# Kernel optimization log

Measured on AMD Instinct MI355X. Metric: run time of the kernel, lower is better.

Reference implementation:

```python
import jax, jax.numpy as jnp
import numpy as np

B, A, N_IN, N_HID, N_OUT, MAX_Z = 2048, 96, 128, 64, 1, 100
SHIFT = float(np.log(2.0))

def ssp(x):
    # shifted softplus: softplus(x) - log(2)
    return jax.nn.softplus(x) - SHIFT

def setup_inputs() -> dict:
    key = jax.random.key(0)
    ks = jax.random.split(key, 8)
    rep = jax.random.normal(ks[0], (B, A, N_IN), dtype=jnp.float32)
    atomic_numbers = jax.random.randint(ks[1], (B, A), 0, MAX_Z)
    atom_mask = jnp.ones((B, A), dtype=jnp.float32)
    s1 = 1.0 / np.sqrt(N_IN)
    s2 = 1.0 / np.sqrt(N_HID)
    W1 = jax.random.uniform(ks[2], (N_IN, N_HID), jnp.float32, -s1, s1)
    b1 = jax.random.uniform(ks[3], (N_HID,), jnp.float32, -s1, s1)
    W2 = jax.random.uniform(ks[4], (N_HID, N_OUT), jnp.float32, -s2, s2)
    b2 = jax.random.uniform(ks[5], (N_OUT,), jnp.float32, -s2, s2)
    atomref_table = jax.random.normal(ks[6], (MAX_Z, N_OUT), dtype=jnp.float32) * 0.1
    atomref_table = atomref_table.at[0].set(0.0)  # mask-atom reference is zero
    mean = jnp.array([0.0], dtype=jnp.float32)
    stddev = jnp.array([1.0], dtype=jnp.float32)
    return {"representation": rep, "atomic_numbers": atomic_numbers,
            "atom_mask": atom_mask, "W1": W1, "b1": b1, "W2": W2, "b2": b2,
            "atomref_table": atomref_table, "mean": mean, "stddev": stddev}

def reference(representation, atomic_numbers, atom_mask, W1, b1, W2, b2,
              atomref_table, mean, stddev):
    # per-atom MLP: [B,A,n_in] -> [B,A,n_out]
    h = ssp(jnp.einsum('bai,ih->bah', representation, W1) + b1)
    yi = jnp.einsum('bah,ho->bao', h, W2) + b2
    # standardize (ScaleShift): y * stddev + mean
    yi = yi * stddev + mean
    # atomref embedding lookup and add
    yi = yi + atomref_table[atomic_numbers]  # [B,A,n_out]
    # masked sum aggregation over atoms (Aggregate axis=1, mean=False)
    y = jnp.sum(yi * atom_mask[..., None], axis=1)  # [B,n_out]
    return y
```

## Files before the change

### kernel.cpp

```cpp
#include <hip/hip_runtime.h>

#define BB 2048
#define AA 96
#define NIN 128
#define NHID 64
#define MI 3

typedef __attribute__((ext_vector_type(8))) short bf16x8;
typedef __attribute__((ext_vector_type(4))) float f32x4;

static __device__ __forceinline__ unsigned f2bf(float x) {
    unsigned u = __builtin_bit_cast(unsigned, x);
    return (u + 0x7FFFu + ((u >> 16) & 1u)) >> 16;
}
static __device__ __forceinline__ unsigned cvt_pk(float a, float b) {
    return f2bf(a) | (f2bf(b) << 16);
}

__global__ __launch_bounds__(256) void atomwise_kernel(
    const float* __restrict__ rep,
    const int*   __restrict__ zs,
    const float* __restrict__ mask,
    const float* __restrict__ w1,
    const float* __restrict__ b1,
    const float* __restrict__ w2,
    const float* __restrict__ b2,
    const float* __restrict__ aref,
    const float* __restrict__ mean,
    const float* __restrict__ stddev,
    float* __restrict__ out)
{
    __shared__ bf16x8 w1f[1024];
    __shared__ float  b1s[NHID], w2s[NHID];

    const int tid  = threadIdx.x;
    const int lane = tid & 63;
    const int wv   = tid >> 6;
    const int nl   = lane & 15;
    const int quad = lane >> 4;

    #pragma unroll
    for (int f = 0; f < 4; ++f) {
        const int fid = tid + f * 256;
        const int l2  = fid & 63;
        const int st  = fid >> 6;
        const int k0  = (st >> 2) * 32 + (l2 >> 4) * 8;
        const int n   = (st & 3) * 16 + (l2 & 15);
        union { bf16x8 v; unsigned u[4]; } fb;
        #pragma unroll
        for (int jp = 0; jp < 4; ++jp)
            fb.u[jp] = cvt_pk(w1[(k0 + 2 * jp) * NHID + n],
                              w1[(k0 + 2 * jp + 1) * NHID + n]);
        w1f[fid] = fb.v;
    }
    if (tid < NHID) { b1s[tid] = b1[tid]; w2s[tid] = w2[tid]; }
    __syncthreads();

    const float sdv  = stddev[0];
    const float cadd = fmaf(b2[0], sdv, mean[0]);
    const float LOG2E = 1.4426950408889634f;
    const float LN2   = 0.6931471805599453f;

    const int wid = blockIdx.x * 4 + wv;

    #pragma unroll 1
    for (int mt = 0; mt < MI; ++mt) {
        const int atom0 = (wid * MI + mt) * 16;
        const float* rowp = rep + (size_t)(atom0 + nl) * NIN + quad * 8;

        f32x4 acc[4];
        #pragma unroll
        for (int t = 0; t < 4; ++t) acc[t] = (f32x4){0.f, 0.f, 0.f, 0.f};

        #pragma unroll 1
        for (int s = 0; s < 4; ++s) {
            const float4 a0 = *(const float4*)(rowp + s * 32);
            const float4 a1 = *(const float4*)(rowp + s * 32 + 4);
            union { bf16x8 v; unsigned u[4]; } fa;
            fa.u[0] = cvt_pk(a0.x, a0.y);
            fa.u[1] = cvt_pk(a0.z, a0.w);
            fa.u[2] = cvt_pk(a1.x, a1.y);
            fa.u[3] = cvt_pk(a1.z, a1.w);
            const bf16x8* fr = &w1f[s * 256 + lane];
            #pragma unroll
            for (int t = 0; t < 4; ++t)
                acc[t] = __builtin_amdgcn_mfma_f32_16x16x32_bf16(fa.v, fr[t * 64], acc[t], 0, 0, 0);
        }

        float v[4];
        #pragma unroll
        for (int r = 0; r < 4; ++r) {
            float p = 0.f;
            #pragma unroll
            for (int t = 0; t < 4; ++t) {
                float x  = acc[t][r] + b1s[t * 16 + nl];
                float ax = fabsf(x);
                float em = exp2f(-ax * LOG2E);
                float sp = fmaxf(x, 0.f) + log2f(1.f + em) * LN2;
                p = fmaf(sp - LN2, w2s[t * 16 + nl], p);
            }
            p += __shfl_xor(p, 1); p += __shfl_xor(p, 2);
            p += __shfl_xor(p, 4); p += __shfl_xor(p, 8);
            v[r] = p;
        }
        if (nl == 0) {
            float ssum = 0.f;
            #pragma unroll
            for (int r = 0; r < 4; ++r) {
                const int ag = atom0 + quad * 4 + r;
                const float yi = fmaf(v[r], sdv, cadd) + aref[zs[ag]];
                ssum += mask[ag] * yi;
            }
            ssum += __shfl_xor(ssum, 16);
            ssum += __shfl_xor(ssum, 32);
            if (lane == 0) atomicAdd(out + atom0 / AA, ssum);
        }
    }
}

extern "C" void kernel_launch(void* const* d_in, const int* in_sizes, int n_in,
                              void* d_out, int out_size, void* d_ws, size_t ws_size,
                              hipStream_t stream) {
    const float* rep    = (const float*)d_in[0];
    const int*   zs     = (const int*)  d_in[1];
    const float* mask   = (const float*)d_in[2];
    const float* w1     = (const float*)d_in[3];
    const float* b1     = (const float*)d_in[4];
    const float* w2     = (const float*)d_in[5];
    const float* b2     = (const float*)d_in[6];
    const float* aref   = (const float*)d_in[7];
    const float* mean   = (const float*)d_in[8];
    const float* stddev = (const float*)d_in[9];
    float* out = (float*)d_out;

    (void)hipMemsetAsync(out, 0, (size_t)out_size * sizeof(float), stream);

    const int atoms  = BB * AA;
    const int blocks = atoms / (4 * 16 * MI);
    atomwise_kernel<<<dim3(blocks), dim3(256), 0, stream>>>(
        rep, zs, mask, w1, b1, w2, b2, aref, mean, stddev, out);
}
```

Measured before the change: 166.1 us.

## Hoist all row loads before MFMA loop, coalesce W1 staging, and use smaller per-wave tile

All eight float4 loads of a 16-atom tile are now issued up front and the K loop is fully unrolled, so the memory latency of the representation reads overlaps instead of being serialized per K step. W1 staging to LDS now reads contiguous float4s and scatters bf16 halves into the fragment layout, replacing strided scalar global reads. MI drops from 3 to 2, so the grid has more blocks and more waves in flight. The cost is more VGPRs for the prefetched rows and a larger share of per-block W1 staging overhead.

```diff
diff --git a/kernel.cpp b/kernel.cpp
--- a/kernel.cpp
+++ b/kernel.cpp
@@ -4,7 +4,7 @@
 #define AA 96
 #define NIN 128
 #define NHID 64
-#define MI 3
+#define MI 2
 
 typedef __attribute__((ext_vector_type(8))) short bf16x8;
 typedef __attribute__((ext_vector_type(4))) float f32x4;
@@ -39,21 +39,26 @@
     const int nl   = lane & 15;
     const int quad = lane >> 4;
 
-    #pragma unroll
-    for (int f = 0; f < 4; ++f) {
-        const int fid = tid + f * 256;
-        const int l2  = fid & 63;
-        const int st  = fid >> 6;
-        const int k0  = (st >> 2) * 32 + (l2 >> 4) * 8;
-        const int n   = (st & 3) * 16 + (l2 & 15);
-        union { bf16x8 v; unsigned u[4]; } fb;
+    {
+        unsigned short* w1h = (unsigned short*)w1f;
+        const float4* w14 = (const float4*)w1;
         #pragma unroll
-        for (int jp = 0; jp < 4; ++jp)
-            fb.u[jp] = cvt_pk(w1[(k0 + 2 * jp) * NHID + n],
-                              w1[(k0 + 2 * jp + 1) * NHID + n]);
-        w1f[fid] = fb.v;
+        for (int i = 0; i < 8; ++i) {
+            const int idx = tid + i * 256;
+            const float4 v = w14[idx];
+            const int k  = idx >> 4;
+            const int n0 = (idx & 15) * 4;
+            const int s = k >> 5, qd = (k >> 3) & 3, jp = (k & 7) >> 1, hf = k & 1;
+            const int t = n0 >> 4;
+            const int base = ((s * 4 + t) * 64 + qd * 16 + (n0 & 15)) * 8 + jp * 2 + hf;
+            w1h[base     ] = (unsigned short)f2bf(v.x);
+            w1h[base +  8] = (unsigned short)f2bf(v.y);
+            w1h[base + 16] = (unsigned short)f2bf(v.z);
+            w1h[base + 24] = (unsigned short)f2bf(v.w);
+        }
+        if (tid < NHID)            b1s[tid] = b1[tid];
+        else if (tid < 2 * NHID)   w2s[tid - NHID] = w2[tid - NHID];
     }
-    if (tid < NHID) { b1s[tid] = b1[tid]; w2s[tid] = w2[tid]; }
     __syncthreads();
 
     const float sdv  = stddev[0];
@@ -68,19 +73,24 @@
         const int atom0 = (wid * MI + mt) * 16;
         const float* rowp = rep + (size_t)(atom0 + nl) * NIN + quad * 8;
 
+        float4 q[8];
+        #pragma unroll
+        for (int s = 0; s < 4; ++s) {
+            q[2 * s]     = *(const float4*)(rowp + s * 32);
+            q[2 * s + 1] = *(const float4*)(rowp + s * 32 + 4);
+        }
+
         f32x4 acc[4];
         #pragma unroll
         for (int t = 0; t < 4; ++t) acc[t] = (f32x4){0.f, 0.f, 0.f, 0.f};
 
-        #pragma unroll 1
+        #pragma unroll
         for (int s = 0; s < 4; ++s) {
-            const float4 a0 = *(const float4*)(rowp + s * 32);
-            const float4 a1 = *(const float4*)(rowp + s * 32 + 4);
             union { bf16x8 v; unsigned u[4]; } fa;
-            fa.u[0] = cvt_pk(a0.x, a0.y);
-            fa.u[1] = cvt_pk(a0.z, a0.w);
-            fa.u[2] = cvt_pk(a1.x, a1.y);
-            fa.u[3] = cvt_pk(a1.z, a1.w);
+            fa.u[0] = cvt_pk(q[2 * s].x,     q[2 * s].y);
+            fa.u[1] = cvt_pk(q[2 * s].z,     q[2 * s].w);
+            fa.u[2] = cvt_pk(q[2 * s + 1].x, q[2 * s + 1].y);
+            fa.u[3] = cvt_pk(q[2 * s + 1].z, q[2 * s + 1].w);
             const bf16x8* fr = &w1f[s * 256 + lane];
             #pragma unroll
             for (int t = 0; t < 4; ++t)
```

After: 173.4 us. +4.4%, slower.
